# Optimization experiments

Hardware: AMD Instinct MI355X
Metric: run time of the kernel (lower is better)

## Reference

```python
import jax, jax.numpy as jnp
import numpy as np

C = 256
NUM_HEADS = 4
NBLK = 6  # 3 stages x depth 2
WS = (2, 8, 8)   # 3D window
SS = (1, 4, 4)   # shift for odd blocks
N_WIN = WS[0] * WS[1] * WS[2]  # 128 tokens per window
RPB_SIZE = (2 * WS[0] - 1) * (2 * WS[1] - 1) * (2 * WS[2] - 1)  # 675


def _rel_index():
    coords = np.stack(np.meshgrid(np.arange(WS[0]), np.arange(WS[1]), np.arange(WS[2]), indexing='ij'))
    coords = coords.reshape(3, -1)
    rel = (coords[:, :, None] - coords[:, None, :]).transpose(1, 2, 0)
    rel[:, :, 0] += WS[0] - 1
    rel[:, :, 1] += WS[1] - 1
    rel[:, :, 2] += WS[2] - 1
    rel[:, :, 0] *= (2 * WS[1] - 1) * (2 * WS[2] - 1)
    rel[:, :, 1] *= (2 * WS[2] - 1)
    return jnp.asarray(rel.sum(-1))  # [N_WIN, N_WIN]

REL_IDX = _rel_index()


def window_partition(x):
    # [B,D,H,W,C] -> [B*nW, N_WIN, C]
    B, D, H, W, Cc = x.shape
    x = x.reshape(B, D // WS[0], WS[0], H // WS[1], WS[1], W // WS[2], WS[2], Cc)
    return x.transpose(0, 1, 3, 5, 2, 4, 6, 7).reshape(-1, N_WIN, Cc)


def window_reverse(win, B, D, H, W):
    Cc = win.shape[-1]
    x = win.reshape(B, D // WS[0], H // WS[1], W // WS[2], WS[0], WS[1], WS[2], Cc)
    return x.transpose(0, 1, 4, 2, 5, 3, 6, 7).reshape(B, D, H, W, Cc)


def attn_mask(D, H, W):
    # standard shifted-window mask, computed on host constants
    img = np.zeros((1, D, H, W, 1), np.float32)
    cnt = 0
    for d in (slice(0, -WS[0]), slice(-WS[0], -SS[0]), slice(-SS[0], None)):
        for h in (slice(0, -WS[1]), slice(-WS[1], -SS[1]), slice(-SS[1], None)):
            for w in (slice(0, -WS[2]), slice(-WS[2], -SS[2]), slice(-SS[2], None)):
                img[:, d, h, w, :] = cnt
                cnt += 1
    mw = img.reshape(1, D // WS[0], WS[0], H // WS[1], WS[1], W // WS[2], WS[2], 1)
    mw = mw.transpose(0, 1, 3, 5, 2, 4, 6, 7).reshape(-1, N_WIN)
    diff = mw[:, None, :] - mw[:, :, None]
    return jnp.asarray(np.where(diff != 0, -100.0, 0.0).astype(np.float32))  # [nW,N,N]


def layer_norm(x, g, b):
    mu = x.mean(-1, keepdims=True)
    var = ((x - mu) ** 2).mean(-1, keepdims=True)
    return (x - mu) * jax.lax.rsqrt(var + 1e-5) * g + b


def setup_inputs() -> dict:
    key = jax.random.key(0)
    ks = jax.random.split(key, 10)
    f = jax.random.normal
    s = 0.02
    return dict(
        x=f(ks[0], (2, 2, 2, 4096, C), jnp.float32),
        n1w=jnp.ones((NBLK, C), jnp.float32), n1b=jnp.zeros((NBLK, C), jnp.float32),
        qkv_w=f(ks[1], (NBLK, C, 3 * C), jnp.float32) * s, qkv_b=jnp.zeros((NBLK, 3 * C), jnp.float32),
        rpb=f(ks[2], (NBLK, RPB_SIZE, NUM_HEADS), jnp.float32) * s,
        proj_w=f(ks[3], (NBLK, C, C), jnp.float32) * s, proj_b=jnp.zeros((NBLK, C), jnp.float32),
        n2w=jnp.ones((NBLK, C), jnp.float32), n2b=jnp.zeros((NBLK, C), jnp.float32),
        mlp1_w=f(ks[4], (NBLK, C, 4 * C), jnp.float32) * s, mlp1_b=jnp.zeros((NBLK, 4 * C), jnp.float32),
        mlp2_w=f(ks[5], (NBLK, 4 * C, C), jnp.float32) * s, mlp2_b=jnp.zeros((NBLK, C), jnp.float32),
        exp_v_w=f(ks[6], (C, 2 * C), jnp.float32) * s,
        exp_v_nw=jnp.ones((C,), jnp.float32), exp_v_nb=jnp.zeros((C,), jnp.float32),
        exp_t_w=f(ks[7], (C, 2 * C), jnp.float32) * s,
        exp_t_nw=jnp.ones((C,), jnp.float32), exp_t_nb=jnp.zeros((C,), jnp.float32),
    )


def reference(x, n1w, n1b, qkv_w, qkv_b, rpb, proj_w, proj_b, n2w, n2b,
              mlp1_w, mlp1_b, mlp2_w, mlp2_b,
              exp_v_w, exp_v_nw, exp_v_nb, exp_t_w, exp_t_nw, exp_t_nb):
    B, T, V, L, _ = x.shape
    H = W = int(round(np.sqrt(L)))
    NH = NUM_HEADS
    dh = C // NH

    def block(h, i, D, shifted, mask):
        # h: [B, D, L, C]
        sc = h
        y = layer_norm(h, n1w[i], n1b[i]).reshape(B, D, H, W, C)
        if shifted:
            y = jnp.roll(y, (-SS[0], -SS[1], -SS[2]), axis=(1, 2, 3))
        win = window_partition(y)  # [B*nW, N, C]
        qkv = (win @ qkv_w[i] + qkv_b[i]).reshape(-1, N_WIN, 3, NH, dh)
        q, k, v = jnp.moveaxis(qkv, 2, 0)              # [B*nW, N, NH, dh]
        q = q.transpose(0, 2, 1, 3)
        k = k.transpose(0, 2, 1, 3)
        v = v.transpose(0, 2, 1, 3)                     # [B*nW, NH, N, dh]
        attn = jnp.einsum('whqd,whkd->whqk', q, k) * (dh ** -0.5)
        attn = attn + rpb[i][REL_IDX].transpose(2, 0, 1)[None]
        if mask is not None:
            nW = mask.shape[0]
            attn = attn.reshape(B, nW, NH, N_WIN, N_WIN) + mask[None, :, None]
            attn = attn.reshape(-1, NH, N_WIN, N_WIN)
        attn = jax.nn.softmax(attn, axis=-1)
        out = jnp.einsum('whqk,whkd->whqd', attn, v).transpose(0, 2, 1, 3).reshape(-1, N_WIN, C)
        out = out @ proj_w[i] + proj_b[i]
        y = window_reverse(out, B, D, H, W)
        if shifted:
            y = jnp.roll(y, (SS[0], SS[1], SS[2]), axis=(1, 2, 3))
        h = sc + y.reshape(B, D, L, C)
        z = layer_norm(h, n2w[i], n2b[i])
        z = jax.nn.gelu(z @ mlp1_w[i] + mlp1_b[i], approximate=False) @ mlp2_w[i] + mlp2_b[i]
        return h + z

    def stage(h, i0, D):
        mask = attn_mask(D, H, W)
        h = block(h, i0, D, False, None)
        h = block(h, i0 + 1, D, True, mask)
        return h

    # stage 1: swin over D = T*V
    h = x.reshape(B, T * V, L, C)
    h = stage(h, 0, T * V)
    h = h.reshape(B, T, V, L, C)

    # stage 2: view patch expand (V -> 2V) + swin
    h = (h @ exp_v_w).reshape(B, T, V, L, 2, C).transpose(0, 1, 2, 4, 3, 5).reshape(B, T, 2 * V, L, C)
    h = layer_norm(h, exp_v_nw, exp_v_nb)
    V2 = 2 * V
    h = h.reshape(B, T * V2, L, C)
    h = stage(h, 2, T * V2)
    h = h.reshape(B, T, V2, L, C)

    # stage 3: temporal patch expand (T -> 2T) + swin
    h = (h @ exp_t_w).reshape(B, T, V2, L, 2, C).transpose(0, 1, 4, 2, 3, 5).reshape(B, 2 * T, V2, L, C)
    h = layer_norm(h, exp_t_nw, exp_t_nb)
    T2 = 2 * T
    h = h.reshape(B, T2 * V2, L, C)
    h = stage(h, 4, T2 * V2)
    return h.reshape(B, T2, V2, L, C)
```

## Files before the change

### kernel.cpp

```cpp
#include <hip/hip_runtime.h>

typedef __bf16 bf16x8 __attribute__((ext_vector_type(8)));
typedef float f32x4 __attribute__((ext_vector_type(4)));
typedef unsigned short u16;
typedef unsigned int u32;

__device__ __forceinline__ u16 f2b(float f) {
    union { float f; u32 u; } v; v.f = f;
    u32 r = v.u + 0x7fffu + ((v.u >> 16) & 1u);
    return (u16)(r >> 16);
}
__device__ __forceinline__ float b2f(u16 u) {
    union { u32 u; float f; } v; v.u = ((u32)u) << 16; return v.f;
}
__device__ __forceinline__ void gl_lds16(const u16* g, u16* l) {
    __builtin_amdgcn_global_load_lds(
        (const __attribute__((address_space(1))) void*)g,
        (__attribute__((address_space(3))) void*)l, 16, 0, 0);
}

__global__ __launch_bounds__(256) void ln_kernel(
    const float* __restrict__ h, u16* __restrict__ out,
    const float* __restrict__ g, const float* __restrict__ bb,
    int D, int dsh, int shifted, int mode)
{
    const int lane = threadIdx.x & 63;
    const int t = blockIdx.x * 4 + (threadIdx.x >> 6);
    const float4 xv = *(const float4*)(h + (size_t)t * 256 + lane * 4);
    float s = xv.x + xv.y + xv.z + xv.w;
    float s2 = xv.x*xv.x + xv.y*xv.y + xv.z*xv.z + xv.w*xv.w;
    #pragma unroll
    for (int o = 32; o > 0; o >>= 1) { s += __shfl_xor(s, o); s2 += __shfl_xor(s2, o); }
    const float mu = s * 0.00390625f;
    const float var = s2 * 0.00390625f - mu * mu;
    const float rs = 1.0f / sqrtf(var + 1e-5f);
    const int c0 = lane * 4;
    const float4 gv = *(const float4*)(g + c0);
    const float4 bv = *(const float4*)(bb + c0);
    ushort4 o4;
    o4.x = f2b((xv.x - mu) * rs * gv.x + bv.x);
    o4.y = f2b((xv.y - mu) * rs * gv.y + bv.y);
    o4.z = f2b((xv.z - mu) * rs * gv.z + bv.z);
    o4.w = f2b((xv.w - mu) * rs * gv.w + bv.w);
    size_t oidx;
    if (mode == 1) {
        oidx = (size_t)t * 256 + c0;
    } else {
        const int b = t >> (dsh + 12);
        const int rem = t & ((1 << (dsh + 12)) - 1);
        int d = rem >> 12;
        const int l = rem & 4095;
        int hh = l >> 6, ww = l & 63;
        if (shifted) { d = d ? d - 1 : D - 1; hh = (hh - 4) & 63; ww = (ww - 4) & 63; }
        const int widx = (b << (dsh + 5)) + ((d >> 1) << 6) + ((hh >> 3) << 3) + (ww >> 3);
        const int n = ((d & 1) << 6) + ((hh & 7) << 3) + (ww & 7);
        oidx = ((size_t)(widx * 128 + n)) * 256 + c0;
    }
    *(ushort4*)(out + oidx) = o4;
}

__global__ __launch_bounds__(256) void cast_kernel(const float* __restrict__ in, u16* __restrict__ out, int n4)
{
    const int i = blockIdx.x * 256 + threadIdx.x;
    if (i >= n4) return;
    const float4 v = ((const float4*)in)[i];
    ushort4 o; o.x = f2b(v.x); o.y = f2b(v.y); o.z = f2b(v.z); o.w = f2b(v.w);
    ((ushort4*)out)[i] = o;
}

__global__ __launch_bounds__(256) void wt_kernel(const float* __restrict__ src, u16* __restrict__ dst, int K, int N)
{
    const size_t base = (size_t)blockIdx.y * K * N;
    const int idx = blockIdx.x * 256 + threadIdx.x;
    const int k = idx / N, n = idx - k * N;
    dst[base + (size_t)n * K + k] = f2b(src[base + idx]);
}

__global__ __launch_bounds__(256) void wt1f_kernel(const float* __restrict__ src, u16* __restrict__ dst)
{
    const size_t base = (size_t)blockIdx.y * 262144;
    const int t = blockIdx.x * 256 + threadIdx.x;
    const int e = t & 7, lane = (t >> 3) & 63, n2 = (t >> 9) & 1, kt = (t >> 10) & 7, c = t >> 13;
    const int k = kt * 32 + (lane >> 4) * 8 + e;
    const int mid = c * 32 + n2 * 16 + (lane & 15);
    dst[base + t] = f2b(src[base + (size_t)k * 1024 + mid]);
}

__global__ __launch_bounds__(256) void wt2f_kernel(const float* __restrict__ src, u16* __restrict__ dst)
{
    const size_t base = (size_t)blockIdx.y * 262144;
    const int t = blockIdx.x * 256 + threadIdx.x;
    const int e = t & 7, lane = (t >> 3) & 63, nt = (t >> 9) & 15, c = t >> 13;
    const int q = lane >> 4;
    const int mid = (e >> 2) * 16 + q * 4 + (e & 3);
    const int k = c * 32 + mid;
    const int out = nt * 16 + (lane & 15);
    dst[base + t] = f2b(src[base + (size_t)k * 256 + out]);
}

struct GemmP {
    const u16* A; const u16* Bt;
    int K;
    const float* bias;
    u16* outb;
    float* outf;
    const float* hin; float* hout;
    int D, shifted, nwsh, row_off;
};

template <int EPI>
__global__ __launch_bounds__(256, 2) void gemm_kernel(GemmP p)
{
    __shared__ __align__(16) char smem[33792];
    float* CF = (float*)smem;

    const int tid = threadIdx.x;
    const int m0 = blockIdx.x * 128, n0 = blockIdx.y * 128;
    const int K = p.K;
    const int lane = tid & 63;
    const int wv = tid >> 6;
    const int wm = (wv & 1) * 64, wn = (wv >> 1) * 64;
    const int l16 = lane & 15, quad = lane >> 4;

    f32x4 acc[4][4];
    #pragma unroll
    for (int a = 0; a < 4; a++)
        #pragma unroll
        for (int b = 0; b < 4; b++)
            acc[a][b] = f32x4{0.f, 0.f, 0.f, 0.f};

    const int lrow = lane >> 2;
    const int c16s = (lane & 3) ^ (lrow & 3);
    const int rA0 = wv * 16;
    const u16* Ag = p.A + (size_t)(m0 + rA0 + lrow) * K + c16s * 8;
    const u16* Bg = p.Bt + (size_t)(n0 + rA0 + lrow) * K + c16s * 8;
    const size_t j64 = (size_t)64 * K;
    const int fslot = (quad ^ (l16 & 3)) * 8;

    {
        u16* Al = (u16*)smem + rA0 * 32;
        u16* Bl = (u16*)(smem + 8192) + rA0 * 32;
        gl_lds16(Ag, Al);
        gl_lds16(Ag + j64, Al + 64 * 32);
        gl_lds16(Bg, Bl);
        gl_lds16(Bg + j64, Bl + 64 * 32);
    }
    __syncthreads();

    int kb = 0;
    for (int k0 = 0; k0 < K; k0 += 32, kb ^= 1) {
        if (k0 + 32 < K) {
            char* nb = smem + (kb ^ 1) * 16384;
            u16* Al = (u16*)nb + rA0 * 32;
            u16* Bl = (u16*)(nb + 8192) + rA0 * 32;
            gl_lds16(Ag + k0 + 32, Al);
            gl_lds16(Ag + j64 + k0 + 32, Al + 64 * 32);
            gl_lds16(Bg + k0 + 32, Bl);
            gl_lds16(Bg + j64 + k0 + 32, Bl + 64 * 32);
        }
        const u16* As = (const u16*)(smem + kb * 16384);
        const u16* Bs = (const u16*)(smem + kb * 16384 + 8192);
        bf16x8 af[4], bfr[4];
        #pragma unroll
        for (int mt = 0; mt < 4; mt++) af[mt] = *(const bf16x8*)(As + (wm + mt * 16 + l16) * 32 + fslot);
        #pragma unroll
        for (int nt = 0; nt < 4; nt++) bfr[nt] = *(const bf16x8*)(Bs + (wn + nt * 16 + l16) * 32 + fslot);
        #pragma unroll
        for (int mt = 0; mt < 4; mt++)
            #pragma unroll
            for (int nt = 0; nt < 4; nt++)
                acc[mt][nt] = __builtin_amdgcn_mfma_f32_16x16x32_bf16(af[mt], bfr[nt], acc[mt][nt], 0, 0, 0);
        __syncthreads();
    }

    const int crow = tid >> 2;
    const int p4 = (tid & 3) * 4;
    #pragma unroll
    for (int c = 0; c < 2; c++) {
        if (c) __syncthreads();
        if ((wv & 1) == c) {
            #pragma unroll
            for (int mt = 0; mt < 4; mt++)
                #pragma unroll
                for (int nt = 0; nt < 4; nt++)
                    #pragma unroll
                    for (int i = 0; i < 4; i++)
                        CF[(mt * 16 + quad * 4 + i) * 132 + wn + nt * 16 + l16] = acc[mt][nt][i];
        }
        __syncthreads();
        const int rowg = m0 + c * 64 + crow;
        size_t tokbase = 0;
        if constexpr (EPI == 1) {
            const int widx = rowg >> 7, n = rowg & 127;
            const int b = widx >> p.nwsh, rem = widx & ((1 << p.nwsh) - 1);
            int dd = ((rem >> 6) << 1) + (n >> 6);
            int hh = (((rem >> 3) & 7) << 3) + ((n >> 3) & 7);
            int ww = ((rem & 7) << 3) + (n & 7);
            if (p.shifted) { dd = (dd + 1 == p.D) ? 0 : dd + 1; hh = (hh + 4) & 63; ww = (ww + 4) & 63; }
            tokbase = ((size_t)((b * p.D + dd) * 4096 + hh * 64 + ww)) * 256;
        } else if constexpr (EPI == 3) {
            tokbase = (size_t)(p.row_off + rowg) * 256;
        }
        #pragma unroll
        for (int j = 0; j < 8; j++) {
            const int colf = j * 16 + p4;
            const int colg = n0 + colf;
            const float4 t = *(const float4*)(CF + crow * 132 + colf);
            const float4 bi = (EPI <= 3) ? *(const float4*)(p.bias + colg) : float4{0.f,0.f,0.f,0.f};
            if constexpr (EPI == 0) {
                const float sc = (colg < 256) ? 0.125f : 1.0f;
                ushort4 pk;
                pk.x = f2b((t.x + bi.x) * sc);
                pk.y = f2b((t.y + bi.y) * sc);
                pk.z = f2b((t.z + bi.z) * sc);
                pk.w = f2b((t.w + bi.w) * sc);
                *(ushort4*)(p.outb + (size_t)rowg * 768 + colg) = pk;
            } else if constexpr (EPI == 1 || EPI == 3) {
                const float* hi = p.hin + tokbase + colg;
                float* ho = p.hout + tokbase + colg;
                const float4 r = *(const float4*)hi;
                float4 o;
                o.x = r.x + t.x + bi.x;
                o.y = r.y + t.y + bi.y;
                o.z = r.z + t.z + bi.z;
                o.w = r.w + t.w + bi.w;
                *(float4*)ho = o;
            } else if constexpr (EPI == 2) {
                float4 g4;
                g4.x = t.x + bi.x; g4.y = t.y + bi.y; g4.z = t.z + bi.z; g4.w = t.w + bi.w;
                ushort4 pk;
                pk.x = f2b(0.5f * g4.x * (1.0f + erff(g4.x * 0.7071067811865475f)));
                pk.y = f2b(0.5f * g4.y * (1.0f + erff(g4.y * 0.7071067811865475f)));
                pk.z = f2b(0.5f * g4.z * (1.0f + erff(g4.z * 0.7071067811865475f)));
                pk.w = f2b(0.5f * g4.w * (1.0f + erff(g4.w * 0.7071067811865475f)));
                *(ushort4*)(p.outb + (size_t)rowg * 1024 + colg) = pk;
            } else {
                *(float4*)(p.outf + (size_t)rowg * 512 + colg) = t;
            }
        }
    }
}

struct MlpP {
    const u16* A;
    const u16* W1t;
    const u16* W2t;
    const float* b1;
    const float* b2;
    const float* hin;
    float* hout;
};

__global__ __launch_bounds__(512, 4) void mlp_fused_kernel(MlpP p)
{
    __shared__ __align__(16) char smem[73728];
    float* CF = (float*)smem;

    const int tid = threadIdx.x;
    const int lane = tid & 63;
    const int wv = tid >> 6;
    const int l16 = lane & 15, quad = lane >> 4;
    const int tok0 = blockIdx.x * 128;
    const int wtok = wv * 16;

    bf16x8 afr[8];
    #pragma unroll
    for (int kt = 0; kt < 8; kt++)
        afr[kt] = *(const bf16x8*)(p.A + (size_t)(tok0 + wtok + l16) * 256 + kt * 32 + quad * 8);

    f32x4 acc2[16];
    #pragma unroll
    for (int nt = 0; nt < 16; nt++) acc2[nt] = f32x4{0.f, 0.f, 0.f, 0.f};

    auto stage = [&](int c) {
        const u16* w1g = p.W1t + (size_t)c * 8192;
        const u16* w2g = p.W2t + (size_t)c * 8192;
        u16* w1b = (u16*)(smem + (c & 1) * 16384);
        u16* w2b = (u16*)(smem + 32768 + (c & 1) * 16384);
        #pragma unroll
        for (int f = 0; f < 2; f++) {
            const int fr = wv * 2 + f;
            gl_lds16(w1g + fr * 512 + lane * 8, w1b + fr * 512);
            gl_lds16(w2g + fr * 512 + lane * 8, w2b + fr * 512);
        }
    };

    stage(0);
    __syncthreads();

    for (int c = 0; c < 32; c++) {
        if (c + 1 < 32) stage(c + 1);

        const u16* W1c = (const u16*)(smem + (c & 1) * 16384);
        f32x4 acc1[2];
        acc1[0] = f32x4{0.f, 0.f, 0.f, 0.f};
        acc1[1] = f32x4{0.f, 0.f, 0.f, 0.f};
        #pragma unroll
        for (int kt = 0; kt < 8; kt++) {
            bf16x8 w1f[2];
            #pragma unroll
            for (int n2 = 0; n2 < 2; n2++)
                w1f[n2] = *(const bf16x8*)(W1c + (kt * 2 + n2) * 512 + lane * 8);
            #pragma unroll
            for (int n2 = 0; n2 < 2; n2++)
                acc1[n2] = __builtin_amdgcn_mfma_f32_16x16x32_bf16(w1f[n2], afr[kt], acc1[n2], 0, 0, 0);
        }

        bf16x8 pa;
        #pragma unroll
        for (int n2 = 0; n2 < 2; n2++) {
            const float4 b1q = *(const float4*)(p.b1 + c * 32 + n2 * 16 + quad * 4);
            #pragma unroll
            for (int i = 0; i < 4; i++) {
                const float b1i = (i == 0) ? b1q.x : (i == 1) ? b1q.y : (i == 2) ? b1q.z : b1q.w;
                const float x = acc1[n2][i] + b1i;
                const float u = x * (1.0f + 0.044715f * x * x);
                const float em = __expf(-1.5957691216f * u);
                const float g = x * __builtin_amdgcn_rcpf(1.0f + em);
                pa[n2 * 4 + i] = (__bf16)g;
            }
        }

        const u16* W2c = (const u16*)(smem + 32768 + (c & 1) * 16384);
        #pragma unroll
        for (int nt = 0; nt < 16; nt++) {
            const bf16x8 w2f = *(const bf16x8*)(W2c + nt * 512 + lane * 8);
            acc2[nt] = __builtin_amdgcn_mfma_f32_16x16x32_bf16(pa, w2f, acc2[nt], 0, 0, 0);
        }
        __syncthreads();
    }

    float b2v[16];
    #pragma unroll
    for (int nt = 0; nt < 16; nt++) b2v[nt] = p.b2[nt * 16 + l16];

    #pragma unroll
    for (int cc = 0; cc < 2; cc++) {
        __syncthreads();
        if ((wv >> 2) == cc) {
            const int rb = (wv & 3) * 16;
            #pragma unroll
            for (int nt = 0; nt < 16; nt++)
                #pragma unroll
                for (int i = 0; i < 4; i++)
                    CF[(rb + quad * 4 + i) * 260 + nt * 16 + l16] = acc2[nt][i] + b2v[nt];
        }
        __syncthreads();
        #pragma unroll
        for (int jj = 0; jj < 8; jj++) {
            const int idx = jj * 512 + tid;
            const int row = idx >> 6, c4 = (idx & 63) << 2;
            const size_t g = (size_t)(tok0 + cc * 64 + row) * 256 + c4;
            const float4 t = *(const float4*)(CF + row * 260 + c4);
            const float4 r = *(const float4*)(p.hin + g);
            float4 o;
            o.x = t.x + r.x; o.y = t.y + r.y; o.z = t.z + r.z; o.w = t.w + r.w;
            *(float4*)(p.hout + g) = o;
        }
    }
}

__global__ __launch_bounds__(256, 2) void attn_mfma_kernel(
    const u16* __restrict__ qkv, u16* __restrict__ att,
    const float* __restrict__ rpbp, int D, int shifted, int w0g, int nwsh)
{
    __shared__ __align__(16) char smem[57856];
    u16* Qs = (u16*)smem;
    u16* Ks = (u16*)(smem + 18432);
    u16* Ps = (u16*)smem;
    u16* Vt = (u16*)(smem + 36864);
    float* rb = (float*)(smem + 54272);
    int* lbl = (int*)(smem + 56972);

    const int wloc = blockIdx.x;
    const int head = blockIdx.y;
    const int tid = threadIdx.x;
    const u16* base = qkv + (size_t)wloc * 98304;

    #pragma unroll
    for (int it = 0; it < 4; it++) {
        const int id = it * 256 + tid;
        const int row = id >> 3, oct = id & 7;
        const size_t ro = (size_t)row * 768 + head * 64 + oct * 8;
        *(uint4*)(Qs + row * 72 + oct * 8) = *(const uint4*)(base + ro);
        *(uint4*)(Ks + row * 72 + oct * 8) = *(const uint4*)(base + ro + 256);
        uint4 vv = *(const uint4*)(base + ro + 512);
        const u16* vp = (const u16*)&vv;
        #pragma unroll
        for (int q = 0; q < 8; q++) Vt[(oct * 8 + q) * 136 + row] = vp[q];
    }
    for (int j = tid; j < 675; j += 256) rb[j] = rpbp[j * 4 + head];
    if (tid < 128) {
        int lv = 0;
        if (shifted) {
            const int widx = w0g + wloc;
            const int rem = widx & ((1 << nwsh) - 1);
            const int d0 = rem >> 6, h0 = (rem >> 3) & 7, w0 = rem & 7;
            const int wd = tid >> 6, wh = (tid >> 3) & 7, ww = tid & 7;
            const int rd = (d0 < (D >> 1) - 1) ? 0 : (1 + wd);
            const int rh = (h0 < 7) ? 0 : (1 + (wh >= 4));
            const int rw = (w0 < 7) ? 0 : (1 + (ww >= 4));
            lv = rd * 9 + rh * 3 + rw;
        }
        lbl[tid] = lv;
    }
    __syncthreads();

    const int wq = tid >> 6;
    const int lane = tid & 63;
    const int l16 = lane & 15, quad = lane >> 4;
    const int myrow0 = wq * 32;

    f32x4 sc[2][8];
    #pragma unroll
    for (int mt = 0; mt < 2; mt++)
        #pragma unroll
        for (int nt = 0; nt < 8; nt++)
            sc[mt][nt] = f32x4{0.f, 0.f, 0.f, 0.f};
    #pragma unroll
    for (int kt = 0; kt < 2; kt++) {
        bf16x8 aq[2];
        #pragma unroll
        for (int mt = 0; mt < 2; mt++)
            aq[mt] = *(const bf16x8*)(Qs + (myrow0 + mt * 16 + l16) * 72 + kt * 32 + quad * 8);
        bf16x8 bk[8];
        #pragma unroll
        for (int nt = 0; nt < 8; nt++)
            bk[nt] = *(const bf16x8*)(Ks + (nt * 16 + l16) * 72 + kt * 32 + quad * 8);
        #pragma unroll
        for (int mt = 0; mt < 2; mt++)
            #pragma unroll
            for (int nt = 0; nt < 8; nt++)
                sc[mt][nt] = __builtin_amdgcn_mfma_f32_16x16x32_bf16(aq[mt], bk[nt], sc[mt][nt], 0, 0, 0);
    }

    float linv[2][4];
    #pragma unroll
    for (int mt = 0; mt < 2; mt++) {
        #pragma unroll
        for (int i = 0; i < 4; i++) {
            const int row = myrow0 + mt * 16 + quad * 4 + i;
            const int rbase = ((row >> 6) + 1) * 225 + (((row >> 3) & 7) + 7) * 15 + ((row & 7) + 7);
            const int lq = lbl[row];
            float mx = -1e30f;
            float sv[8];
            #pragma unroll
            for (int nt = 0; nt < 8; nt++) {
                const int col = nt * 16 + l16;
                float v = sc[mt][nt][i] + rb[rbase - (col >> 6) * 225 - ((col >> 3) & 7) * 15 - (col & 7)];
                if (shifted && lq != lbl[col]) v -= 100.0f;
                sv[nt] = v;
                mx = fmaxf(mx, v);
            }
            #pragma unroll
            for (int o = 1; o < 16; o <<= 1) mx = fmaxf(mx, __shfl_xor(mx, o));
            float l = 0.0f;
            #pragma unroll
            for (int nt = 0; nt < 8; nt++) {
                const float pp = __expf(sv[nt] - mx);
                sc[mt][nt][i] = pp;
                l += pp;
            }
            #pragma unroll
            for (int o = 1; o < 16; o <<= 1) l += __shfl_xor(l, o);
            linv[mt][i] = 1.0f / l;
        }
    }

    __syncthreads();
    #pragma unroll
    for (int mt = 0; mt < 2; mt++)
        #pragma unroll
        for (int nt = 0; nt < 8; nt++)
            #pragma unroll
            for (int i = 0; i < 4; i++)
                Ps[(myrow0 + mt * 16 + quad * 4 + i) * 136 + nt * 16 + l16] = f2b(sc[mt][nt][i]);

    f32x4 oc[2][4];
    #pragma unroll
    for (int mt = 0; mt < 2; mt++)
        #pragma unroll
        for (int nt = 0; nt < 4; nt++)
            oc[mt][nt] = f32x4{0.f, 0.f, 0.f, 0.f};
    #pragma unroll
    for (int kt = 0; kt < 4; kt++) {
        bf16x8 ap[2];
        #pragma unroll
        for (int mt = 0; mt < 2; mt++)
            ap[mt] = *(const bf16x8*)(Ps + (myrow0 + mt * 16 + l16) * 136 + kt * 32 + quad * 8);
        bf16x8 bv[4];
        #pragma unroll
        for (int nt = 0; nt < 4; nt++)
            bv[nt] = *(const bf16x8*)(Vt + (nt * 16 + l16) * 136 + kt * 32 + quad * 8);
        #pragma unroll
        for (int mt = 0; mt < 2; mt++)
            #pragma unroll
            for (int nt = 0; nt < 4; nt++)
                oc[mt][nt] = __builtin_amdgcn_mfma_f32_16x16x32_bf16(ap[mt], bv[nt], oc[mt][nt], 0, 0, 0);
    }

    #pragma unroll
    for (int mt = 0; mt < 2; mt++)
        #pragma unroll
        for (int nt = 0; nt < 4; nt++)
            #pragma unroll
            for (int i = 0; i < 4; i++) {
                const int row = myrow0 + mt * 16 + quad * 4 + i;
                const int col = nt * 16 + l16;
                att[(size_t)(wloc * 128 + row) * 256 + head * 64 + col] = f2b(oc[mt][nt][i] * linv[mt][i]);
            }
}

__global__ __launch_bounds__(256) void expand_ln_kernel(
    const float* __restrict__ sc, float* __restrict__ hout,
    const float* __restrict__ g, const float* __restrict__ bb,
    int it0, int typ)
{
    const int lane = threadIdx.x & 63;
    const int ot = blockIdx.x * 4 + (threadIdx.x >> 6);
    const int itl = ot >> 1, e = ot & 1;
    const float4 xv = *(const float4*)(sc + (size_t)itl * 512 + e * 256 + lane * 4);
    float s = xv.x + xv.y + xv.z + xv.w;
    float s2 = xv.x*xv.x + xv.y*xv.y + xv.z*xv.z + xv.w*xv.w;
    #pragma unroll
    for (int o = 32; o > 0; o >>= 1) { s += __shfl_xor(s, o); s2 += __shfl_xor(s2, o); }
    const float mu = s * 0.00390625f;
    const float var = s2 * 0.00390625f - mu * mu;
    const float rs = 1.0f / sqrtf(var + 1e-5f);
    const int c0 = lane * 4;
    const float4 gv = *(const float4*)(g + c0);
    const float4 bv = *(const float4*)(bb + c0);
    float4 y;
    y.x = (xv.x - mu) * rs * gv.x + bv.x;
    y.y = (xv.y - mu) * rs * gv.y + bv.y;
    y.z = (xv.z - mu) * rs * gv.z + bv.z;
    y.w = (xv.w - mu) * rs * gv.w + bv.w;
    const int it = it0 + itl;
    size_t otg;
    if (typ == 0) {
        const int b = it >> 14, rr = it & 16383;
        const int t = rr >> 13, v = (rr >> 12) & 1, l = rr & 4095;
        otg = (size_t)(((b * 2 + t) * 4 + v * 2 + e) * 4096 + l);
    } else {
        const int b = it >> 15, rr = it & 32767;
        const int t = rr >> 14, v2 = (rr >> 12) & 3, l = rr & 4095;
        otg = (size_t)(((b * 4 + t * 2 + e) * 4 + v2) * 4096 + l);
    }
    *(float4*)(hout + otg * 256 + c0) = y;
}

extern "C" void kernel_launch(void* const* d_in, const int* in_sizes, int n_in,
                              void* d_out, int out_size, void* d_ws, size_t ws_size,
                              hipStream_t stream)
{
    const float* x      = (const float*)d_in[0];
    const float* n1w    = (const float*)d_in[1];
    const float* n1b    = (const float*)d_in[2];
    const float* qkv_w  = (const float*)d_in[3];
    const float* qkv_b  = (const float*)d_in[4];
    const float* rpb    = (const float*)d_in[5];
    const float* proj_w = (const float*)d_in[6];
    const float* proj_b = (const float*)d_in[7];
    const float* n2w    = (const float*)d_in[8];
    const float* n2b    = (const float*)d_in[9];
    const float* mlp1_w = (const float*)d_in[10];
    const float* mlp1_b = (const float*)d_in[11];
    const float* mlp2_w = (const float*)d_in[12];
    const float* mlp2_b = (const float*)d_in[13];
    const float* expv_w = (const float*)d_in[14];
    const float* expv_nw= (const float*)d_in[15];
    const float* expv_nb= (const float*)d_in[16];
    const float* expt_w = (const float*)d_in[17];
    const float* expt_nw= (const float*)d_in[18];
    const float* expt_nb= (const float*)d_in[19];
    (void)in_sizes; (void)n_in; (void)out_size;

    if (ws_size < 352321536ULL) return;

    char* ws = (char*)d_ws;
    float* h    = (float*)ws;
    u16*  winb  = (u16*)(ws + 134217728LL);
    u16*  att   = (u16*)(ws + 134217728LL + 67108864LL);
    char* scr   = ws + 134217728LL + 2LL * 67108864LL;
    u16*  scrb  = (u16*)scr;
    float* scrf = (float*)scr;
    u16* qkvT   = (u16*)(ws + 134217728LL + 3LL * 67108864LL);
    u16* projT  = qkvT + 6 * 768 * 256;
    u16* mlp1T  = projT + 6 * 256 * 256;
    u16* mlp2T  = mlp1T + 6 * 1024 * 256;
    u16* expvT  = mlp2T + 6 * 256 * 1024;
    u16* exptT  = expvT + 512 * 256;

    wt_kernel<<<dim3(768, 6), 256, 0, stream>>>(qkv_w, qkvT, 256, 768);
    wt_kernel<<<dim3(256, 6), 256, 0, stream>>>(proj_w, projT, 256, 256);
    wt1f_kernel<<<dim3(1024, 6), 256, 0, stream>>>(mlp1_w, mlp1T);
    wt2f_kernel<<<dim3(1024, 6), 256, 0, stream>>>(mlp2_w, mlp2T);
    wt_kernel<<<dim3(512, 1), 256, 0, stream>>>(expv_w, expvT, 256, 512);
    wt_kernel<<<dim3(512, 1), 256, 0, stream>>>(expt_w, exptT, 256, 512);
    hipMemcpyAsync(h, x, 33554432ULL, hipMemcpyDeviceToDevice, stream);

    for (int s = 0; s < 3; s++) {
        const int D = 4 << s;
        const int dsh = 2 + s;
        const int nwsh = dsh + 5;
        const int tokens = 2 * D * 4096;
        const int nch = tokens / 32768;
        for (int j = 0; j < 2; j++) {
            const int i = 2 * s + j;
            ln_kernel<<<dim3(tokens / 4), 256, 0, stream>>>(h, winb, n1w + i * 256, n1b + i * 256, D, dsh, j, 0);
            for (int c = 0; c < nch; c++) {
                GemmP gq{};
                gq.A = winb + (size_t)c * 32768 * 256;
                gq.Bt = qkvT + (size_t)i * 768 * 256;
                gq.K = 256; gq.bias = qkv_b + i * 768; gq.outb = scrb;
                gemm_kernel<0><<<dim3(256, 6), 256, 0, stream>>>(gq);
                attn_mfma_kernel<<<dim3(256, 4), 256, 0, stream>>>(scrb, att + (size_t)c * 32768 * 256,
                                                                   rpb + i * 675 * 4, D, j, c * 256, nwsh);
            }
            GemmP gp{};
            gp.A = att; gp.Bt = projT + (size_t)i * 256 * 256; gp.K = 256;
            gp.bias = proj_b + i * 256; gp.hin = h; gp.hout = h;
            gp.D = D; gp.shifted = j; gp.nwsh = nwsh;
            gemm_kernel<1><<<dim3(tokens / 128, 2), 256, 0, stream>>>(gp);
            ln_kernel<<<dim3(tokens / 4), 256, 0, stream>>>(h, winb, n2w + i * 256, n2b + i * 256, D, dsh, 0, 1);
            MlpP mp{};
            mp.A = winb;
            mp.W1t = mlp1T + (size_t)i * 262144;
            mp.W2t = mlp2T + (size_t)i * 262144;
            mp.b1 = mlp1_b + i * 1024;
            mp.b2 = mlp2_b + i * 256;
            mp.hin = h;
            mp.hout = (s == 2 && j == 1) ? (float*)d_out : h;
            mlp_fused_kernel<<<dim3(tokens / 128), 512, 0, stream>>>(mp);
        }
        if (s < 2) {
            const int ntok = tokens;
            cast_kernel<<<dim3(ntok * 64 / 256), 256, 0, stream>>>(h, winb, ntok * 64);
            const u16* eT = (s == 0) ? expvT : exptT;
            const float* eg = (s == 0) ? expv_nw : expt_nw;
            const float* eb = (s == 0) ? expv_nb : expt_nb;
            for (int c = 0; c < ntok / 32768; c++) {
                GemmP ge{};
                ge.A = winb + (size_t)c * 32768 * 256; ge.Bt = eT; ge.K = 256; ge.outf = scrf;
                gemm_kernel<4><<<dim3(256, 4), 256, 0, stream>>>(ge);
                expand_ln_kernel<<<dim3(16384), 256, 0, stream>>>(scrf, h, eg, eb, c * 32768, s);
            }
        }
    }
}
```

Measured before the change: 2.413 ms.

## Retile fused MLP waves to 32 tokens x half outputs; swap GEMM grid order

In the fused MLP kernel, each wave now handles 32 tokens (two 16-row groups) and half of the output columns instead of 16 tokens and all columns. Each W1/W2 fragment read from LDS therefore feeds two MFMAs, which cuts LDS traffic per FLOP. The cost is that the first GEMM and the GELU work are duplicated across the wave pair. Separately, the generic GEMM grid is transposed so that adjacent blocks share the same A row tile across N tiles, which should improve L2 reuse of the activations.

```diff
diff --git a/kernel.cpp b/kernel.cpp
--- a/kernel.cpp
+++ b/kernel.cpp
@@ -115,7 +115,7 @@
     float* CF = (float*)smem;
 
     const int tid = threadIdx.x;
-    const int m0 = blockIdx.x * 128, n0 = blockIdx.y * 128;
+    const int m0 = blockIdx.y * 128, n0 = blockIdx.x * 128;
     const int K = p.K;
     const int lane = tid & 63;
     const int wv = tid >> 6;
@@ -253,24 +253,30 @@
 
 __global__ __launch_bounds__(512, 4) void mlp_fused_kernel(MlpP p)
 {
-    __shared__ __align__(16) char smem[73728];
+    __shared__ __align__(16) char smem[66560];
     float* CF = (float*)smem;
 
     const int tid = threadIdx.x;
     const int lane = tid & 63;
     const int wv = tid >> 6;
+    const int tg = wv >> 1, oh = wv & 1;
     const int l16 = lane & 15, quad = lane >> 4;
     const int tok0 = blockIdx.x * 128;
-    const int wtok = wv * 16;
-
-    bf16x8 afr[8];
-    #pragma unroll
-    for (int kt = 0; kt < 8; kt++)
-        afr[kt] = *(const bf16x8*)(p.A + (size_t)(tok0 + wtok + l16) * 256 + kt * 32 + quad * 8);
-
-    f32x4 acc2[16];
-    #pragma unroll
-    for (int nt = 0; nt < 16; nt++) acc2[nt] = f32x4{0.f, 0.f, 0.f, 0.f};
+    const int wtok = tg * 32;
+
+    bf16x8 afr[2][8];
+    #pragma unroll
+    for (int g = 0; g < 2; g++)
+        #pragma unroll
+        for (int kt = 0; kt < 8; kt++)
+            afr[g][kt] = *(const bf16x8*)(p.A + (size_t)(tok0 + wtok + g * 16 + l16) * 256 + kt * 32 + quad * 8);
+
+    f32x4 acc2[2][8];
+    #pragma unroll
+    for (int g = 0; g < 2; g++)
+        #pragma unroll
+        for (int nt = 0; nt < 8; nt++)
+            acc2[g][nt] = f32x4{0.f, 0.f, 0.f, 0.f};
 
     auto stage = [&](int c) {
         const u16* w1g = p.W1t + (size_t)c * 8192;
@@ -292,9 +298,12 @@
         if (c + 1 < 32) stage(c + 1);
 
         const u16* W1c = (const u16*)(smem + (c & 1) * 16384);
-        f32x4 acc1[2];
-        acc1[0] = f32x4{0.f, 0.f, 0.f, 0.f};
-        acc1[1] = f32x4{0.f, 0.f, 0.f, 0.f};
+        f32x4 acc1[2][2];
+        #pragma unroll
+        for (int g = 0; g < 2; g++)
+            #pragma unroll
+            for (int n2 = 0; n2 < 2; n2++)
+                acc1[g][n2] = f32x4{0.f, 0.f, 0.f, 0.f};
         #pragma unroll
         for (int kt = 0; kt < 8; kt++) {
             bf16x8 w1f[2];
@@ -302,48 +311,57 @@
             for (int n2 = 0; n2 < 2; n2++)
                 w1f[n2] = *(const bf16x8*)(W1c + (kt * 2 + n2) * 512 + lane * 8);
             #pragma unroll
-            for (int n2 = 0; n2 < 2; n2++)
-                acc1[n2] = __builtin_amdgcn_mfma_f32_16x16x32_bf16(w1f[n2], afr[kt], acc1[n2], 0, 0, 0);
-        }
-
-        bf16x8 pa;
+            for (int g = 0; g < 2; g++)
+                #pragma unroll
+                for (int n2 = 0; n2 < 2; n2++)
+                    acc1[g][n2] = __builtin_amdgcn_mfma_f32_16x16x32_bf16(w1f[n2], afr[g][kt], acc1[g][n2], 0, 0, 0);
+        }
+
+        bf16x8 pa[2];
         #pragma unroll
         for (int n2 = 0; n2 < 2; n2++) {
             const float4 b1q = *(const float4*)(p.b1 + c * 32 + n2 * 16 + quad * 4);
             #pragma unroll
             for (int i = 0; i < 4; i++) {
                 const float b1i = (i == 0) ? b1q.x : (i == 1) ? b1q.y : (i == 2) ? b1q.z : b1q.w;
-                const float x = acc1[n2][i] + b1i;
-                const float u = x * (1.0f + 0.044715f * x * x);
-                const float em = __expf(-1.5957691216f * u);
-                const float g = x * __builtin_amdgcn_rcpf(1.0f + em);
-                pa[n2 * 4 + i] = (__bf16)g;
+                #pragma unroll
+                for (int g = 0; g < 2; g++) {
+                    const float x = acc1[g][n2][i] + b1i;
+                    const float u = x * (1.0f + 0.044715f * x * x);
+                    const float em = __expf(-1.5957691216f * u);
+                    const float gv = x * __builtin_amdgcn_rcpf(1.0f + em);
+                    pa[g][n2 * 4 + i] = (__bf16)gv;
+                }
             }
         }
 
         const u16* W2c = (const u16*)(smem + 32768 + (c & 1) * 16384);
         #pragma unroll
-        for (int nt = 0; nt < 16; nt++) {
-            const bf16x8 w2f = *(const bf16x8*)(W2c + nt * 512 + lane * 8);
-            acc2[nt] = __builtin_amdgcn_mfma_f32_16x16x32_bf16(pa, w2f, acc2[nt], 0, 0, 0);
+        for (int nt = 0; nt < 8; nt++) {
+            const bf16x8 w2f = *(const bf16x8*)(W2c + (oh * 8 + nt) * 512 + lane * 8);
+            #pragma unroll
+            for (int g = 0; g < 2; g++)
+                acc2[g][nt] = __builtin_amdgcn_mfma_f32_16x16x32_bf16(pa[g], w2f, acc2[g][nt], 0, 0, 0);
         }
         __syncthreads();
     }
 
-    float b2v[16];
-    #pragma unroll
-    for (int nt = 0; nt < 16; nt++) b2v[nt] = p.b2[nt * 16 + l16];
+    float b2v[8];
+    #pragma unroll
+    for (int nt = 0; nt < 8; nt++) b2v[nt] = p.b2[oh * 128 + nt * 16 + l16];
 
     #pragma unroll
     for (int cc = 0; cc < 2; cc++) {
         __syncthreads();
         if ((wv >> 2) == cc) {
-            const int rb = (wv & 3) * 16;
-            #pragma unroll
-            for (int nt = 0; nt < 16; nt++)
+            const int rb = (tg & 1) * 32;
+            #pragma unroll
+            for (int g = 0; g < 2; g++)
                 #pragma unroll
-                for (int i = 0; i < 4; i++)
-                    CF[(rb + quad * 4 + i) * 260 + nt * 16 + l16] = acc2[nt][i] + b2v[nt];
+                for (int nt = 0; nt < 8; nt++)
+                    #pragma unroll
+                    for (int i = 0; i < 4; i++)
+                        CF[(rb + g * 16 + quad * 4 + i) * 260 + oh * 128 + nt * 16 + l16] = acc2[g][nt][i] + b2v[nt];
         }
         __syncthreads();
         #pragma unroll
@@ -613,7 +631,7 @@
                 gq.A = winb + (size_t)c * 32768 * 256;
                 gq.Bt = qkvT + (size_t)i * 768 * 256;
                 gq.K = 256; gq.bias = qkv_b + i * 768; gq.outb = scrb;
-                gemm_kernel<0><<<dim3(256, 6), 256, 0, stream>>>(gq);
+                gemm_kernel<0><<<dim3(6, 256), 256, 0, stream>>>(gq);
                 attn_mfma_kernel<<<dim3(256, 4), 256, 0, stream>>>(scrb, att + (size_t)c * 32768 * 256,
                                                                    rpb + i * 675 * 4, D, j, c * 256, nwsh);
             }
@@ -621,7 +639,7 @@
             gp.A = att; gp.Bt = projT + (size_t)i * 256 * 256; gp.K = 256;
             gp.bias = proj_b + i * 256; gp.hin = h; gp.hout = h;
             gp.D = D; gp.shifted = j; gp.nwsh = nwsh;
-            gemm_kernel<1><<<dim3(tokens / 128, 2), 256, 0, stream>>>(gp);
+            gemm_kernel<1><<<dim3(2, tokens / 128), 256, 0, stream>>>(gp);
             ln_kernel<<<dim3(tokens / 4), 256, 0, stream>>>(h, winb, n2w + i * 256, n2b + i * 256, D, dsh, 0, 1);
             MlpP mp{};
             mp.A = winb;
@@ -642,7 +660,7 @@
             for (int c = 0; c < ntok / 32768; c++) {
                 GemmP ge{};
                 ge.A = winb + (size_t)c * 32768 * 256; ge.Bt = eT; ge.K = 256; ge.outf = scrf;
-                gemm_kernel<4><<<dim3(256, 4), 256, 0, stream>>>(ge);
+                gemm_kernel<4><<<dim3(4, 256), 256, 0, stream>>>(ge);
                 expand_ln_kernel<<<dim3(16384), 256, 0, stream>>>(scrf, h, eg, eb, c * 32768, s);
             }
         }
```

Result: slower. 3.529 ms (+46.3%).

## Widen GEMM tile to 128x256 so each A tile feeds twice the columns

Applied to the files above, without the earlier changes.

The generic GEMM kernel now computes a 128x256 output tile per block instead of 128x128. Each wave holds two sets of 4x4 accumulators, the B tile in shared memory doubles, and the epilogue writes out 32 rows per pass. The grids in all GEMM launches are halved in the N dimension. The aim is to load each A tile from global memory once per 256 columns. The cost is 128 accumulator registers per thread and 48KB of shared memory, which may reduce occupancy under launch_bounds(256,2), and fewer blocks in the grid.

```diff
diff --git a/kernel.cpp b/kernel.cpp
--- a/kernel.cpp
+++ b/kernel.cpp
@@ -111,101 +111,92 @@
 template <int EPI>
 __global__ __launch_bounds__(256, 2) void gemm_kernel(GemmP p)
 {
-    __shared__ __align__(16) char smem[33792];
+    __shared__ __align__(16) char smem[49152];
     float* CF = (float*)smem;
 
     const int tid = threadIdx.x;
-    const int m0 = blockIdx.x * 128, n0 = blockIdx.y * 128;
+    const int m0 = blockIdx.x * 128, n0 = blockIdx.y * 256;
     const int K = p.K;
     const int lane = tid & 63;
     const int wv = tid >> 6;
     const int wm = (wv & 1) * 64, wn = (wv >> 1) * 64;
     const int l16 = lane & 15, quad = lane >> 4;
 
-    f32x4 acc[4][4];
-    #pragma unroll
-    for (int a = 0; a < 4; a++)
-        #pragma unroll
-        for (int b = 0; b < 4; b++)
-            acc[a][b] = f32x4{0.f, 0.f, 0.f, 0.f};
+    f32x4 acc[2][4][4];
+    #pragma unroll
+    for (int pn = 0; pn < 2; pn++)
+        #pragma unroll
+        for (int a = 0; a < 4; a++)
+            #pragma unroll
+            for (int b = 0; b < 4; b++)
+                acc[pn][a][b] = f32x4{0.f, 0.f, 0.f, 0.f};
 
     const int lrow = lane >> 2;
     const int c16s = (lane & 3) ^ (lrow & 3);
-    const int rA0 = wv * 16;
-    const u16* Ag = p.A + (size_t)(m0 + rA0 + lrow) * K + c16s * 8;
-    const u16* Bg = p.Bt + (size_t)(n0 + rA0 + lrow) * K + c16s * 8;
+    const u16* Ag = p.A + (size_t)(m0 + wv * 16 + lrow) * K + c16s * 8;
+    const u16* Bg = p.Bt + (size_t)(n0 + wv * 64 + lrow) * K + c16s * 8;
     const size_t j64 = (size_t)64 * K;
     const int fslot = (quad ^ (l16 & 3)) * 8;
 
-    {
-        u16* Al = (u16*)smem + rA0 * 32;
-        u16* Bl = (u16*)(smem + 8192) + rA0 * 32;
-        gl_lds16(Ag, Al);
-        gl_lds16(Ag + j64, Al + 64 * 32);
-        gl_lds16(Bg, Bl);
-        gl_lds16(Bg + j64, Bl + 64 * 32);
-    }
+    auto stage = [&](int kb, int k0) {
+        u16* Al = (u16*)(smem + kb * 24576) + (wv * 16) * 32;
+        u16* Bl = (u16*)(smem + kb * 24576 + 8192) + (wv * 64) * 32;
+        gl_lds16(Ag + k0, Al);
+        gl_lds16(Ag + j64 + k0, Al + 64 * 32);
+        #pragma unroll
+        for (int f = 0; f < 4; f++)
+            gl_lds16(Bg + (size_t)(f * 16) * K + k0, Bl + f * 16 * 32);
+    };
+
+    stage(0, 0);
     __syncthreads();
 
     int kb = 0;
     for (int k0 = 0; k0 < K; k0 += 32, kb ^= 1) {
-        if (k0 + 32 < K) {
-            char* nb = smem + (kb ^ 1) * 16384;
-            u16* Al = (u16*)nb + rA0 * 32;
-            u16* Bl = (u16*)(nb + 8192) + rA0 * 32;
-            gl_lds16(Ag + k0 + 32, Al);
-            gl_lds16(Ag + j64 + k0 + 32, Al + 64 * 32);
-            gl_lds16(Bg + k0 + 32, Bl);
-            gl_lds16(Bg + j64 + k0 + 32, Bl + 64 * 32);
-        }
-        const u16* As = (const u16*)(smem + kb * 16384);
-        const u16* Bs = (const u16*)(smem + kb * 16384 + 8192);
-        bf16x8 af[4], bfr[4];
+        if (k0 + 32 < K) stage(kb ^ 1, k0 + 32);
+        const u16* As = (const u16*)(smem + kb * 24576);
+        const u16* Bs = (const u16*)(smem + kb * 24576 + 8192);
+        bf16x8 af[4];
         #pragma unroll
         for (int mt = 0; mt < 4; mt++) af[mt] = *(const bf16x8*)(As + (wm + mt * 16 + l16) * 32 + fslot);
         #pragma unroll
-        for (int nt = 0; nt < 4; nt++) bfr[nt] = *(const bf16x8*)(Bs + (wn + nt * 16 + l16) * 32 + fslot);
-        #pragma unroll
-        for (int mt = 0; mt < 4; mt++)
+        for (int pn = 0; pn < 2; pn++) {
+            bf16x8 bfr[4];
             #pragma unroll
             for (int nt = 0; nt < 4; nt++)
-                acc[mt][nt] = __builtin_amdgcn_mfma_f32_16x16x32_bf16(af[mt], bfr[nt], acc[mt][nt], 0, 0, 0);
-        __syncthreads();
-    }
-
-    const int crow = tid >> 2;
-    const int p4 = (tid & 3) * 4;
-    #pragma unroll
-    for (int c = 0; c < 2; c++) {
-        if (c) __syncthreads();
-        if ((wv & 1) == c) {
+                bfr[nt] = *(const bf16x8*)(Bs + (pn * 128 + wn + nt * 16 + l16) * 32 + fslot);
             #pragma unroll
             for (int mt = 0; mt < 4; mt++)
                 #pragma unroll
                 for (int nt = 0; nt < 4; nt++)
+                    acc[pn][mt][nt] = __builtin_amdgcn_mfma_f32_16x16x32_bf16(af[mt], bfr[nt], acc[pn][mt][nt], 0, 0, 0);
+        }
+        __syncthreads();
+    }
+
+    #pragma unroll
+    for (int cc = 0; cc < 4; cc++) {
+        if (cc) __syncthreads();
+        if ((wv & 1) == (cc >> 1)) {
+            const int mb = (cc & 1) * 2;
+            #pragma unroll
+            for (int pn = 0; pn < 2; pn++)
+                #pragma unroll
+                for (int mtl = 0; mtl < 2; mtl++)
                     #pragma unroll
-                    for (int i = 0; i < 4; i++)
-                        CF[(mt * 16 + quad * 4 + i) * 132 + wn + nt * 16 + l16] = acc[mt][nt][i];
+                    for (int nt = 0; nt < 4; nt++)
+                        #pragma unroll
+                        for (int i = 0; i < 4; i++)
+                            CF[(mtl * 16 + quad * 4 + i) * 264 + pn * 128 + wn + nt * 16 + l16] = acc[pn][mb + mtl][nt][i];
         }
         __syncthreads();
-        const int rowg = m0 + c * 64 + crow;
-        size_t tokbase = 0;
-        if constexpr (EPI == 1) {
-            const int widx = rowg >> 7, n = rowg & 127;
-            const int b = widx >> p.nwsh, rem = widx & ((1 << p.nwsh) - 1);
-            int dd = ((rem >> 6) << 1) + (n >> 6);
-            int hh = (((rem >> 3) & 7) << 3) + ((n >> 3) & 7);
-            int ww = ((rem & 7) << 3) + (n & 7);
-            if (p.shifted) { dd = (dd + 1 == p.D) ? 0 : dd + 1; hh = (hh + 4) & 63; ww = (ww + 4) & 63; }
-            tokbase = ((size_t)((b * p.D + dd) * 4096 + hh * 64 + ww)) * 256;
-        } else if constexpr (EPI == 3) {
-            tokbase = (size_t)(p.row_off + rowg) * 256;
-        }
-        #pragma unroll
-        for (int j = 0; j < 8; j++) {
-            const int colf = j * 16 + p4;
-            const int colg = n0 + colf;
-            const float4 t = *(const float4*)(CF + crow * 132 + colf);
+        #pragma unroll
+        for (int jj = 0; jj < 8; jj++) {
+            const int idx = jj * 256 + tid;
+            const int row = idx >> 6, c4 = (idx & 63) << 2;
+            const int rowg = m0 + cc * 32 + row;
+            const int colg = n0 + c4;
+            const float4 t = *(const float4*)(CF + row * 264 + c4);
             const float4 bi = (EPI <= 3) ? *(const float4*)(p.bias + colg) : float4{0.f,0.f,0.f,0.f};
             if constexpr (EPI == 0) {
                 const float sc = (colg < 256) ? 0.125f : 1.0f;
@@ -216,6 +207,18 @@
                 pk.w = f2b((t.w + bi.w) * sc);
                 *(ushort4*)(p.outb + (size_t)rowg * 768 + colg) = pk;
             } else if constexpr (EPI == 1 || EPI == 3) {
+                size_t tokbase;
+                if constexpr (EPI == 1) {
+                    const int widx = rowg >> 7, n = rowg & 127;
+                    const int b = widx >> p.nwsh, rem = widx & ((1 << p.nwsh) - 1);
+                    int dd = ((rem >> 6) << 1) + (n >> 6);
+                    int hh = (((rem >> 3) & 7) << 3) + ((n >> 3) & 7);
+                    int ww = ((rem & 7) << 3) + (n & 7);
+                    if (p.shifted) { dd = (dd + 1 == p.D) ? 0 : dd + 1; hh = (hh + 4) & 63; ww = (ww + 4) & 63; }
+                    tokbase = ((size_t)((b * p.D + dd) * 4096 + hh * 64 + ww)) * 256;
+                } else {
+                    tokbase = (size_t)(p.row_off + rowg) * 256;
+                }
                 const float* hi = p.hin + tokbase + colg;
                 float* ho = p.hout + tokbase + colg;
                 const float4 r = *(const float4*)hi;
@@ -613,7 +616,7 @@
                 gq.A = winb + (size_t)c * 32768 * 256;
                 gq.Bt = qkvT + (size_t)i * 768 * 256;
                 gq.K = 256; gq.bias = qkv_b + i * 768; gq.outb = scrb;
-                gemm_kernel<0><<<dim3(256, 6), 256, 0, stream>>>(gq);
+                gemm_kernel<0><<<dim3(256, 3), 256, 0, stream>>>(gq);
                 attn_mfma_kernel<<<dim3(256, 4), 256, 0, stream>>>(scrb, att + (size_t)c * 32768 * 256,
                                                                    rpb + i * 675 * 4, D, j, c * 256, nwsh);
             }
@@ -621,7 +624,7 @@
             gp.A = att; gp.Bt = projT + (size_t)i * 256 * 256; gp.K = 256;
             gp.bias = proj_b + i * 256; gp.hin = h; gp.hout = h;
             gp.D = D; gp.shifted = j; gp.nwsh = nwsh;
-            gemm_kernel<1><<<dim3(tokens / 128, 2), 256, 0, stream>>>(gp);
+            gemm_kernel<1><<<dim3(tokens / 128, 1), 256, 0, stream>>>(gp);
             ln_kernel<<<dim3(tokens / 4), 256, 0, stream>>>(h, winb, n2w + i * 256, n2b + i * 256, D, dsh, 0, 1);
             MlpP mp{};
             mp.A = winb;
@@ -642,7 +645,7 @@
             for (int c = 0; c < ntok / 32768; c++) {
                 GemmP ge{};
                 ge.A = winb + (size_t)c * 32768 * 256; ge.Bt = eT; ge.K = 256; ge.outf = scrf;
-                gemm_kernel<4><<<dim3(256, 4), 256, 0, stream>>>(ge);
+                gemm_kernel<4><<<dim3(256, 2), 256, 0, stream>>>(ge);
                 expand_ln_kernel<<<dim3(16384), 256, 0, stream>>>(scrf, h, eg, eb, c * 32768, s);
             }
         }
```

Measured after the change: 2.440 ms. About the same (+1.1%).
